# Performance work log

Measured on AMD Instinct MI355X. Metric: run time of the kernel, lower is better.

The kernel has to match this reference:

```python
import math
import jax, jax.numpy as jnp
import numpy as np

B, NH, L0 = 16, 128, 16384
KS, STRIDE = 4, 2
INIT_GATE_BIAS = 1.0


def _num_steps(L, ks, stride):
    # number of reduce steps until any N <= L reaches N <= 1 (matches torch N recurrence)
    d, n = 0, L
    while True:
        n = (max(n - ks, 0) + stride - 1) // stride + 1
        d += 1
        if n <= 1:
            return d


def setup_inputs() -> dict:
    key = jax.random.key(0)
    k1, k2, k3, k4 = jax.random.split(key, 4)
    h = jax.random.normal(k1, (B, NH, L0), dtype=jnp.float32)
    N = jax.random.randint(k2, (B,), 1, L0 + 1, dtype=jnp.int32)
    cin = NH + 1  # depth_variant adds one channel
    bound = 1.0 / math.sqrt(cin * KS)
    W = jax.random.uniform(k3, (3 * NH, cin, KS), minval=-bound, maxval=bound, dtype=jnp.float32)
    b = jax.random.uniform(k4, (3 * NH,), minval=-bound, maxval=bound, dtype=jnp.float32)
    b = b.at[2 * NH:].set(INIT_GATE_BIAS)
    return {"h": h, "N": N, "W": W, "b": b}


def _step(h, N, depth, W, b):
    Bb, _, Lc = h.shape
    # depth channel (depth_variant=True), then mask invalid positions (mask applied after concat, as in torch)
    d = jnp.full((Bb, 1, Lc), math.log1p(depth), dtype=h.dtype)
    hh = jnp.concatenate([h, d], axis=1)
    mask = (jnp.arange(Lc) < N[:, None]).astype(hh.dtype)  # [B, Lc]
    hh = hh * mask[:, None, :]
    # right-pad so conv covers all valid positions
    if Lc < KS:
        pad_r = KS - Lc
    elif (Lc - KS) % STRIDE != 0:
        pad_r = STRIDE - (Lc - KS) % STRIDE
    else:
        pad_r = 0
    if pad_r:
        hh = jnp.pad(hh, ((0, 0), (0, 0), (0, pad_r)))
    lrg = jax.lax.conv_general_dilated(
        hh, W, window_strides=(STRIDE,), padding='VALID',
        dimension_numbers=('NCH', 'OIH', 'NCH')) + b[None, :, None]
    l = lrg[:, :NH]
    r = jnp.tanh(lrg[:, NH:2 * NH])
    g = jax.nn.sigmoid(lrg[:, 2 * NH:])
    h_new = l * g + r * (1.0 - g)
    m = jnp.maximum(N - KS, 0)
    N_new = (m + STRIDE - 1) // STRIDE + 1  # ceil(clamp(N-ks,0)/stride)+1
    return h_new, N_new


def reference(h, N, W, b):
    # Fixed-depth unroll: instead of compacting the batch (dynamic shapes), run
    # every sample for all D steps and record its row at the step it finishes.
    # Torch output order = samples sorted stably by finish depth (boolean-index
    # compaction preserves original relative order), reproduced via stable argsort.
    D = _num_steps(h.shape[2], KS, STRIDE)
    Bb = h.shape[0]
    out_h = jnp.zeros((Bb, NH), dtype=h.dtype)
    finish = jnp.full((Bb,), D, dtype=jnp.int32)
    done = jnp.zeros((Bb,), dtype=bool)
    for depth in range(D):
        h, N = _step(h, N, depth, W, b)
        newly = (~done) & (N <= 1)
        out_h = jnp.where(newly[:, None], h[:, :, 0], out_h)
        finish = jnp.where(newly, depth, finish)
        done = done | newly
    order = jnp.argsort(finish)  # stable by default in jax
    return out_h[order]
```

## Files before the change

### kernel.cpp

```cpp
#include <hip/hip_runtime.h>
#include <math.h>

typedef _Float16 f16_t;
typedef _Float16 f16x8 __attribute__((ext_vector_type(8)));
typedef _Float16 f16x4 __attribute__((ext_vector_type(4)));
typedef float    f32x4 __attribute__((ext_vector_type(4)));

#define NHC 128
#define NBATCH 16
#define JT 64
#define THREADS 512
#define LDSROWPITCH 272
#define LDSREGION (66*LDSROWPITCH)

__device__ __host__ __forceinline__ int nstep_f(int n){ int m = n - 4; m = m < 0 ? 0 : m; return ((m + 1) >> 1) + 1; }

__global__ void prep_kernel(const float* __restrict__ W, const float* __restrict__ bin,
                            f16_t* __restrict__ Wt, float* __restrict__ Pp, float* __restrict__ biasf)
{
    int c = blockIdx.x;
    int i = threadIdx.x;
    #pragma unroll
    for (int k = 0; k < 4; k++)
        Wt[((size_t)k*384 + c)*128 + i] = (f16_t)W[((size_t)c*129 + i)*4 + k];
    if (i == 0) {
        float s = 0.f;
        Pp[c*5 + 0] = 0.f;
        #pragma unroll
        for (int k = 0; k < 4; k++) { s += W[((size_t)c*129 + 128)*4 + k]; Pp[c*5 + k + 1] = s; }
        biasf[c] = bin[c];
    }
}

__global__ void transpose_kernel(const float* __restrict__ h, const int* __restrict__ N0,
                                 f16_t* __restrict__ X0, int outCols)
{
    __shared__ float tile[32][65];
    const int b = blockIdx.z, c0 = blockIdx.y*32, p0 = blockIdx.x*64;
    const int tid = threadIdx.x;
    const int n0 = N0[b];
    const int L0c = 16384;
    {
        int c = tid >> 3, pc = (tid & 7) * 8;
        const float* src = h + ((size_t)b*NHC + c0 + c)*L0c + p0 + pc;
        float4 v0 = *(const float4*)(src);
        float4 v1 = *(const float4*)(src + 4);
        *(float4*)(&tile[c][pc])     = v0;
        *(float4*)(&tile[c][pc + 4]) = v1;
    }
    __syncthreads();
    {
        int p = tid >> 2, cc = (tid & 3) * 8;
        bool dead = (p0 + p >= n0);
        f16x8 vv;
        #pragma unroll
        for (int e = 0; e < 8; e++) vv[e] = dead ? (f16_t)0.f : (f16_t)tile[cc + e][p];
        *(f16x8*)(X0 + ((size_t)b*outCols + p0 + p)*NHC + c0 + cc) = vv;
    }
}

template<bool TO_LDS>
__device__ __forceinline__ void gemm_epilogue(
    const char* ldsIn, char* ldsOut, f16_t* goutB,
    const f16_t* __restrict__ Wt, const float* __restrict__ Pp,
    const float* __restrict__ biasf, float* __restrict__ outrow,
    int j0, int Nt, int Nt1, float dval, bool record)
{
    const int tid  = threadIdx.x;
    const int w    = tid >> 6;
    const int lane = tid & 63;
    const int n16  = lane & 15;
    const int q    = lane >> 4;

    f32x4 acc[3][4] = {};

    const int arow = w*16 + n16;
    #pragma unroll 1
    for (int k = 0; k < 4; k++) {
        const char*  bb0 = ldsIn + (k&1)*LDSREGION + ((k>>1) + n16)*LDSROWPITCH + q*16;
        const f16_t* ab  = Wt + ((size_t)k*384 + arow)*128 + q*8;
        #pragma unroll 1
        for (int kc = 0; kc < 4; kc++) {
            f16x8 a0 = *(const f16x8*)(ab + kc*32);
            f16x8 a1 = *(const f16x8*)(ab + 16384 + kc*32);
            f16x8 a2 = *(const f16x8*)(ab + 32768 + kc*32);
            #pragma unroll
            for (int ct = 0; ct < 4; ct++) {
                f16x8 bb = *(const f16x8*)(bb0 + ct*(16*LDSROWPITCH) + kc*64);
                acc[0][ct] = __builtin_amdgcn_mfma_f32_16x16x32_f16(a0, bb, acc[0][ct], 0, 0, 0);
                acc[1][ct] = __builtin_amdgcn_mfma_f32_16x16x32_f16(a1, bb, acc[1][ct], 0, 0, 0);
                acc[2][ct] = __builtin_amdgcn_mfma_f32_16x16x32_f16(a2, bb, acc[2][ct], 0, 0, 0);
            }
        }
    }

    if constexpr (TO_LDS) __syncthreads();

    const int cw = w*16 + q*4;
    float biasr[3][4], pfull[3][4];
    #pragma unroll
    for (int s = 0; s < 3; s++)
        #pragma unroll
        for (int r = 0; r < 4; r++) {
            int row = s*128 + cw + r;
            biasr[s][r] = biasf[row];
            pfull[s][r] = Pp[row*5 + 4];
        }

    #pragma unroll
    for (int ct = 0; ct < 4; ct++) {
        int j = j0 + ct*16 + n16;
        int cnt = Nt - 2*j; cnt = cnt < 0 ? 0 : (cnt > 4 ? 4 : cnt);
        bool zero = (j >= Nt1);
        float hv[4];
        #pragma unroll
        for (int r = 0; r < 4; r++) {
            float d0, d1, d2;
            if (cnt == 4)      { d0 = pfull[0][r]; d1 = pfull[1][r]; d2 = pfull[2][r]; }
            else if (cnt == 0) { d0 = 0.f; d1 = 0.f; d2 = 0.f; }
            else { int rw = cw + r; d0 = Pp[rw*5 + cnt]; d1 = Pp[(128+rw)*5 + cnt]; d2 = Pp[(256+rw)*5 + cnt]; }
            float lv = acc[0][ct][r] + biasr[0][r] + dval*d0;
            float rp = acc[1][ct][r] + biasr[1][r] + dval*d1;
            float gp = acc[2][ct][r] + biasr[2][r] + dval*d2;
            float e2 = __expf(2.f*rp);
            float rv = 1.f - 2.f/(e2 + 1.f);
            float gv = 1.f/(1.f + __expf(-gp));
            float hh = lv*gv + rv*(1.f - gv);
            hv[r] = zero ? 0.f : hh;
        }
        f16x4 hb;
        #pragma unroll
        for (int r = 0; r < 4; r++) hb[r] = (f16_t)hv[r];
        if constexpr (TO_LDS) {
            *(f16x4*)(ldsOut + (j&1)*LDSREGION + (j>>1)*LDSROWPITCH + cw*2) = hb;
        } else {
            *(f16x4*)(goutB + (ct*16 + n16)*NHC + cw) = hb;
        }
        if (record && ct == 0 && n16 == 0) {
            #pragma unroll
            for (int r = 0; r < 4; r++) outrow[cw + r] = hv[r];
        }
    }
}

__global__ __launch_bounds__(THREADS) void conv_kernel(
    const f16_t* __restrict__ Xin, f16_t* __restrict__ Xout,
    const f16_t* __restrict__ Wt, const float* __restrict__ Pp,
    const float* __restrict__ biasf, const int* __restrict__ N0,
    float* __restrict__ outbuf,
    int t, int inCols, int outCols, float dval)
{
    __shared__ alignas(16) char ldsX[2*LDSREGION];
    const int b  = blockIdx.y;
    const int j0 = blockIdx.x * JT;
    const int tid = threadIdx.x;
    int Nt = N0[b];
    for (int s = 0; s < t; s++) Nt = nstep_f(Nt);
    const int Nt1 = nstep_f(Nt);

    f16_t* XoutB = Xout + ((size_t)b*outCols + j0)*NHC;
    if (j0 >= Nt1) {
        float4 z = {0.f,0.f,0.f,0.f};
        float4* p = (float4*)XoutB;
        #pragma unroll
        for (int i = 0; i < 2; i++) p[i*THREADS + tid] = z;
        return;
    }

    const char* XinB = (const char*)(Xin + ((size_t)b*inCols + 2*(size_t)j0)*NHC);
    const int maxrow = inCols - 2*j0;
    for (int it = 0; it < 5; ++it) {
        int idx = it*THREADS + tid;
        if (idx < 130*16) {
            int row = idx >> 4, cb = (idx & 15) * 16;
            float4 v = {0.f,0.f,0.f,0.f};
            if (row < maxrow) v = *(const float4*)(XinB + row*256 + cb);
            *(float4*)(ldsX + (row&1)*LDSREGION + (row>>1)*LDSROWPITCH + cb) = v;
        }
    }
    __syncthreads();

    bool newly = (Nt1 == 1) && (t == 0 || Nt > 1);
    gemm_epilogue<false>(ldsX, nullptr, XoutB, Wt, Pp, biasf, outbuf + b*NHC,
                         j0, Nt, Nt1, dval, newly && (j0 == 0));
}

__global__ __launch_bounds__(THREADS) void tail_kernel(
    const f16_t* __restrict__ Xin, const f16_t* __restrict__ Wt,
    const float* __restrict__ Pp, const float* __restrict__ biasf,
    const int* __restrict__ N0, float* __restrict__ outbuf, int inCols)
{
    __shared__ alignas(16) char ldsX[2*LDSREGION];
    const int b = blockIdx.x;
    const int tid = threadIdx.x;
    int Nt = N0[b];
    for (int s = 0; s < 7; s++) Nt = nstep_f(Nt);

    const char* XinB = (const char*)(Xin + (size_t)b*inCols*NHC);
    for (int it = 0; it < 5; ++it) {
        int idx = it*THREADS + tid;
        if (idx < 130*16) {
            int row = idx >> 4, cb = (idx & 15) * 16;
            float4 v = {0.f,0.f,0.f,0.f};
            if (row < inCols) v = *(const float4*)(XinB + row*256 + cb);
            *(float4*)(ldsX + (row&1)*LDSREGION + (row>>1)*LDSROWPITCH + cb) = v;
        }
    }
    __syncthreads();

    for (int t = 7; t < 13; ++t) {
        int Nt1 = nstep_f(Nt);
        bool newly = (Nt1 == 1) && (Nt > 1);
        float dval = log1pf((float)t);
        gemm_epilogue<true>(ldsX, ldsX, nullptr, Wt, Pp, biasf, outbuf + b*NHC,
                            0, Nt, Nt1, dval, newly);
        Nt = Nt1;
        __syncthreads();
    }
}

__global__ void finalize_kernel(const float* __restrict__ outbuf,
                                const int* __restrict__ N0, float* __restrict__ dout)
{
    __shared__ int fin[16];
    __shared__ int rnk[16];
    int tid = threadIdx.x;
    if (tid < 16) {
        int n = N0[tid]; int f = 12;
        for (int t = 0; t < 13; t++) { n = nstep_f(n); if (n == 1) { f = t; break; } }
        fin[tid] = f;
    }
    __syncthreads();
    if (tid < 16) {
        int r = 0;
        for (int b2 = 0; b2 < 16; b2++)
            if (fin[b2] < fin[tid] || (fin[b2] == fin[tid] && b2 < tid)) r++;
        rnk[tid] = r;
    }
    __syncthreads();
    for (int e = tid; e < NBATCH*NHC; e += 256) {
        int b = e >> 7, c = e & 127;
        dout[rnk[b]*NHC + c] = outbuf[e];
    }
}

extern "C" void kernel_launch(void* const* d_in, const int* in_sizes, int n_in,
                              void* d_out, int out_size, void* d_ws, size_t ws_size,
                              hipStream_t stream)
{
    const float* h    = (const float*)d_in[0];
    const int*   N0   = (const int*)d_in[1];
    const float* W    = (const float*)d_in[2];
    const float* bvec = (const float*)d_in[3];
    float* dout = (float*)d_out;

    int Ls[14], Ms[14];
    Ls[0] = 16384;
    for (int t = 0; t < 13; t++) Ls[t+1] = nstep_f(Ls[t]);
    for (int t = 0; t < 14; t++) Ms[t] = ((Ls[t] + 63) / 64) * 64;

    char* ws = (char*)d_ws;
    size_t off = 0;
    auto alloc = [&](size_t bytes){ size_t o = off; off += (bytes + 255) & ~(size_t)255; return o; };
    size_t oXA   = alloc((size_t)NBATCH * Ms[0] * NHC * 2);
    size_t oXB   = alloc((size_t)NBATCH * Ms[1] * NHC * 2);
    size_t oWt   = alloc((size_t)4*384*128*2);
    size_t oPp   = alloc((size_t)384*5*4);
    size_t oBias = alloc((size_t)384*4);
    size_t oOut  = alloc((size_t)NBATCH*NHC*4);
    f16_t* XA    = (f16_t*)(ws + oXA);
    f16_t* XB    = (f16_t*)(ws + oXB);
    f16_t* Wt    = (f16_t*)(ws + oWt);
    float* Pp    = (float*)(ws + oPp);
    float* biasf = (float*)(ws + oBias);
    float* outb  = (float*)(ws + oOut);

    hipLaunchKernelGGL(prep_kernel, dim3(384), dim3(128), 0, stream, W, bvec, Wt, Pp, biasf);
    hipLaunchKernelGGL(transpose_kernel, dim3(Ms[0]/64, 4, NBATCH), dim3(256), 0, stream, h, N0, XA, Ms[0]);

    f16_t* cur = XA; f16_t* nxt = XB;
    for (int t = 0; t < 7; t++) {
        hipLaunchKernelGGL(conv_kernel, dim3(Ms[t+1]/64, NBATCH), dim3(THREADS), 0, stream,
                           cur, nxt, Wt, Pp, biasf, N0, outb, t, Ms[t], Ms[t+1], log1pf((float)t));
        f16_t* tmp = cur; cur = nxt; nxt = tmp;
    }
    hipLaunchKernelGGL(tail_kernel, dim3(NBATCH), dim3(THREADS), 0, stream,
                       cur, Wt, Pp, biasf, N0, outb, Ms[7]);
    hipLaunchKernelGGL(finalize_kernel, dim3(1), dim3(256), 0, stream, outb, N0, dout);
}
```

Before: 524.9 us.

## Specialize tail kernel with column-tile-count templated MFMA loop and early exits

Replaces the generic gemm_epilogue call in the tail kernel with a dedicated tail_iter templated on the number of active 16-column tiles, chosen from the shrinking sequence length each step. Blocks whose sample is already finished return immediately, and blocks exit once their sample finishes. Bias and full-window depth projections are hoisted into registers. This cuts MFMA work on columns that are already dead in the late, short steps, at the cost of more code paths and template instantiations.

```diff
diff --git a/kernel.cpp b/kernel.cpp
--- a/kernel.cpp
+++ b/kernel.cpp
@@ -185,6 +185,68 @@
                          j0, Nt, Nt1, dval, newly && (j0 == 0));
 }
 
+template<int CTM>
+__device__ __forceinline__ void tail_iter(
+    char* ldsX, const f16_t* __restrict__ Wt, const float* __restrict__ Pp,
+    float* __restrict__ outrow,
+    const float (&biasr)[3][4], const float (&pfull)[3][4],
+    int n16, int q, int arow, int cw,
+    int Nt, int Nt1, float dval, bool newly)
+{
+    f32x4 acc[3][CTM] = {};
+    #pragma unroll
+    for (int k = 0; k < 4; k++) {
+        const char*  bb0 = ldsX + (k&1)*LDSREGION + ((k>>1) + n16)*LDSROWPITCH + q*16;
+        const f16_t* ab  = Wt + ((size_t)k*384 + arow)*128 + q*8;
+        #pragma unroll
+        for (int kc = 0; kc < 4; kc++) {
+            f16x8 a0 = *(const f16x8*)(ab + kc*32);
+            f16x8 a1 = *(const f16x8*)(ab + 16384 + kc*32);
+            f16x8 a2 = *(const f16x8*)(ab + 32768 + kc*32);
+            #pragma unroll
+            for (int ct = 0; ct < CTM; ct++) {
+                f16x8 bb = *(const f16x8*)(bb0 + ct*(16*LDSROWPITCH) + kc*64);
+                acc[0][ct] = __builtin_amdgcn_mfma_f32_16x16x32_f16(a0, bb, acc[0][ct], 0, 0, 0);
+                acc[1][ct] = __builtin_amdgcn_mfma_f32_16x16x32_f16(a1, bb, acc[1][ct], 0, 0, 0);
+                acc[2][ct] = __builtin_amdgcn_mfma_f32_16x16x32_f16(a2, bb, acc[2][ct], 0, 0, 0);
+            }
+        }
+    }
+
+    __syncthreads();
+
+    #pragma unroll
+    for (int ct = 0; ct < CTM; ct++) {
+        int j = ct*16 + n16;
+        int cnt = Nt - 2*j; cnt = cnt < 0 ? 0 : (cnt > 4 ? 4 : cnt);
+        bool zero = (j >= Nt1);
+        float hv[4];
+        #pragma unroll
+        for (int r = 0; r < 4; r++) {
+            float d0, d1, d2;
+            if (cnt == 4)      { d0 = pfull[0][r]; d1 = pfull[1][r]; d2 = pfull[2][r]; }
+            else if (cnt == 0) { d0 = 0.f; d1 = 0.f; d2 = 0.f; }
+            else { int rw = cw + r; d0 = Pp[rw*5 + cnt]; d1 = Pp[(128+rw)*5 + cnt]; d2 = Pp[(256+rw)*5 + cnt]; }
+            float lv = acc[0][ct][r] + biasr[0][r] + dval*d0;
+            float rp = acc[1][ct][r] + biasr[1][r] + dval*d1;
+            float gp = acc[2][ct][r] + biasr[2][r] + dval*d2;
+            float e2 = __expf(2.f*rp);
+            float rv = 1.f - 2.f/(e2 + 1.f);
+            float gv = 1.f/(1.f + __expf(-gp));
+            float hh = lv*gv + rv*(1.f - gv);
+            hv[r] = zero ? 0.f : hh;
+        }
+        f16x4 hb;
+        #pragma unroll
+        for (int r = 0; r < 4; r++) hb[r] = (f16_t)hv[r];
+        *(f16x4*)(ldsX + (j&1)*LDSREGION + (j>>1)*LDSROWPITCH + cw*2) = hb;
+        if (newly && ct == 0 && n16 == 0) {
+            #pragma unroll
+            for (int r = 0; r < 4; r++) outrow[cw + r] = hv[r];
+        }
+    }
+}
+
 __global__ __launch_bounds__(THREADS) void tail_kernel(
     const f16_t* __restrict__ Xin, const f16_t* __restrict__ Wt,
     const float* __restrict__ Pp, const float* __restrict__ biasf,
@@ -195,6 +257,7 @@
     const int tid = threadIdx.x;
     int Nt = N0[b];
     for (int s = 0; s < 7; s++) Nt = nstep_f(Nt);
+    if (Nt <= 1) return;
 
     const char* XinB = (const char*)(Xin + (size_t)b*inCols*NHC);
     for (int it = 0; it < 5; ++it) {
@@ -206,14 +269,38 @@
             *(float4*)(ldsX + (row&1)*LDSREGION + (row>>1)*LDSROWPITCH + cb) = v;
         }
     }
+
+    const int w    = tid >> 6;
+    const int lane = tid & 63;
+    const int n16  = lane & 15;
+    const int q    = lane >> 4;
+    const int arow = w*16 + n16;
+    const int cw   = w*16 + q*4;
+    float* outrow  = outbuf + b*NHC;
+
+    float biasr[3][4], pfull[3][4];
+    #pragma unroll
+    for (int s = 0; s < 3; s++)
+        #pragma unroll
+        for (int r = 0; r < 4; r++) {
+            int row = s*128 + cw + r;
+            biasr[s][r] = biasf[row];
+            pfull[s][r] = Pp[row*5 + 4];
+        }
     __syncthreads();
 
     for (int t = 7; t < 13; ++t) {
         int Nt1 = nstep_f(Nt);
-        bool newly = (Nt1 == 1) && (Nt > 1);
+        bool newly = (Nt1 == 1);
         float dval = log1pf((float)t);
-        gemm_epilogue<true>(ldsX, ldsX, nullptr, Wt, Pp, biasf, outbuf + b*NHC,
-                            0, Nt, Nt1, dval, newly);
+        int ctmax = (Nt1 >> 4) + 1; if (ctmax > 4) ctmax = 4;
+        switch (ctmax) {
+        case 1:  tail_iter<1>(ldsX, Wt, Pp, outrow, biasr, pfull, n16, q, arow, cw, Nt, Nt1, dval, newly); break;
+        case 2:  tail_iter<2>(ldsX, Wt, Pp, outrow, biasr, pfull, n16, q, arow, cw, Nt, Nt1, dval, newly); break;
+        case 3:  tail_iter<3>(ldsX, Wt, Pp, outrow, biasr, pfull, n16, q, arow, cw, Nt, Nt1, dval, newly); break;
+        default: tail_iter<4>(ldsX, Wt, Pp, outrow, biasr, pfull, n16, q, arow, cw, Nt, Nt1, dval, newly); break;
+        }
+        if (newly) return;
         Nt = Nt1;
         __syncthreads();
     }
```

Result: faster. 512.8 us (-2.3%).

## Hoist weight fragments into registers and skip MFMA tiles past valid length

Applied to the files above, without the earlier changes.

Loads all A-matrix weight fragments (48 f16x8 vectors per thread) into registers once per block before the LDS fill, instead of reloading them from global memory inside the k-loop. The GEMM is templated on the number of active column tiles, so tiles beyond the sample's current valid length are not computed, in both the step kernel and the tail kernel. The tail kernel also returns early for samples that are already finished and exits once a sample finishes. The cost is much higher register pressure (about 192 VGPRs for the A fragments plus accumulators), which may limit occupancy or cause spills, and more code from the template variants.

```diff
diff --git a/kernel.cpp b/kernel.cpp
--- a/kernel.cpp
+++ b/kernel.cpp
@@ -59,45 +59,26 @@
     }
 }
 
-template<bool TO_LDS>
-__device__ __forceinline__ void gemm_epilogue(
-    const char* ldsIn, char* ldsOut, f16_t* goutB,
-    const f16_t* __restrict__ Wt, const float* __restrict__ Pp,
-    const float* __restrict__ biasf, float* __restrict__ outrow,
-    int j0, int Nt, int Nt1, float dval, bool record)
-{
-    const int tid  = threadIdx.x;
-    const int w    = tid >> 6;
-    const int lane = tid & 63;
-    const int n16  = lane & 15;
-    const int q    = lane >> 4;
-
-    f32x4 acc[3][4] = {};
-
-    const int arow = w*16 + n16;
-    #pragma unroll 1
+struct AFrag { f16x8 a[4][4][3]; };
+
+__device__ __forceinline__ void load_afrag(AFrag& A, const f16_t* __restrict__ Wt, int arow, int q)
+{
+    #pragma unroll
     for (int k = 0; k < 4; k++) {
-        const char*  bb0 = ldsIn + (k&1)*LDSREGION + ((k>>1) + n16)*LDSROWPITCH + q*16;
-        const f16_t* ab  = Wt + ((size_t)k*384 + arow)*128 + q*8;
-        #pragma unroll 1
+        const f16_t* ab = Wt + ((size_t)k*384 + arow)*128 + q*8;
+        #pragma unroll
         for (int kc = 0; kc < 4; kc++) {
-            f16x8 a0 = *(const f16x8*)(ab + kc*32);
-            f16x8 a1 = *(const f16x8*)(ab + 16384 + kc*32);
-            f16x8 a2 = *(const f16x8*)(ab + 32768 + kc*32);
-            #pragma unroll
-            for (int ct = 0; ct < 4; ct++) {
-                f16x8 bb = *(const f16x8*)(bb0 + ct*(16*LDSROWPITCH) + kc*64);
-                acc[0][ct] = __builtin_amdgcn_mfma_f32_16x16x32_f16(a0, bb, acc[0][ct], 0, 0, 0);
-                acc[1][ct] = __builtin_amdgcn_mfma_f32_16x16x32_f16(a1, bb, acc[1][ct], 0, 0, 0);
-                acc[2][ct] = __builtin_amdgcn_mfma_f32_16x16x32_f16(a2, bb, acc[2][ct], 0, 0, 0);
-            }
-        }
-    }
-
-    if constexpr (TO_LDS) __syncthreads();
-
-    const int cw = w*16 + q*4;
-    float biasr[3][4], pfull[3][4];
+            A.a[k][kc][0] = *(const f16x8*)(ab + kc*32);
+            A.a[k][kc][1] = *(const f16x8*)(ab + 16384 + kc*32);
+            A.a[k][kc][2] = *(const f16x8*)(ab + 32768 + kc*32);
+        }
+    }
+}
+
+__device__ __forceinline__ void load_biasp(float (&biasr)[3][4], float (&pfull)[3][4],
+                                           const float* __restrict__ biasf,
+                                           const float* __restrict__ Pp, int cw)
+{
     #pragma unroll
     for (int s = 0; s < 3; s++)
         #pragma unroll
@@ -106,9 +87,37 @@
             biasr[s][r] = biasf[row];
             pfull[s][r] = Pp[row*5 + 4];
         }
-
-    #pragma unroll
-    for (int ct = 0; ct < 4; ct++) {
+}
+
+template<int CTM>
+__device__ __forceinline__ void gemm_regA(f32x4 (&acc)[3][4], const AFrag& A,
+                                          const char* ldsIn, int n16, int q)
+{
+    #pragma unroll
+    for (int k = 0; k < 4; k++) {
+        const char* bb0 = ldsIn + (k&1)*LDSREGION + ((k>>1) + n16)*LDSROWPITCH + q*16;
+        #pragma unroll
+        for (int kc = 0; kc < 4; kc++) {
+            #pragma unroll
+            for (int ct = 0; ct < CTM; ct++) {
+                f16x8 bb = *(const f16x8*)(bb0 + ct*(16*LDSROWPITCH) + kc*64);
+                acc[0][ct] = __builtin_amdgcn_mfma_f32_16x16x32_f16(A.a[k][kc][0], bb, acc[0][ct], 0, 0, 0);
+                acc[1][ct] = __builtin_amdgcn_mfma_f32_16x16x32_f16(A.a[k][kc][1], bb, acc[1][ct], 0, 0, 0);
+                acc[2][ct] = __builtin_amdgcn_mfma_f32_16x16x32_f16(A.a[k][kc][2], bb, acc[2][ct], 0, 0, 0);
+            }
+        }
+    }
+}
+
+template<int CTE, bool TO_LDS>
+__device__ __forceinline__ void epilogue_store(
+    const f32x4 (&acc)[3][4], char* ldsOut, f16_t* goutB,
+    const float (&biasr)[3][4], const float (&pfull)[3][4],
+    const float* __restrict__ Pp, float* __restrict__ outrow,
+    int j0, int Nt, int Nt1, float dval, bool record, int n16, int cw)
+{
+    #pragma unroll
+    for (int ct = 0; ct < CTE; ct++) {
         int j = j0 + ct*16 + n16;
         int cnt = Nt - 2*j; cnt = cnt < 0 ? 0 : (cnt > 4 ? 4 : cnt);
         bool zero = (j >= Nt1);
@@ -167,6 +176,18 @@
         return;
     }
 
+    const int w    = tid >> 6;
+    const int lane = tid & 63;
+    const int n16  = lane & 15;
+    const int q    = lane >> 4;
+    const int arow = w*16 + n16;
+    const int cw   = w*16 + q*4;
+
+    AFrag A;
+    load_afrag(A, Wt, arow, q);
+    float biasr[3][4], pfull[3][4];
+    load_biasp(biasr, pfull, biasf, Pp, cw);
+
     const char* XinB = (const char*)(Xin + ((size_t)b*inCols + 2*(size_t)j0)*NHC);
     const int maxrow = inCols - 2*j0;
     for (int it = 0; it < 5; ++it) {
@@ -180,9 +201,32 @@
     }
     __syncthreads();
 
+    f32x4 acc[3][4] = {};
+    int ctm = (Nt1 - j0 + 15) >> 4; if (ctm > 4) ctm = 4;
+    switch (ctm) {
+    case 1:  gemm_regA<1>(acc, A, ldsX, n16, q); break;
+    case 2:  gemm_regA<2>(acc, A, ldsX, n16, q); break;
+    case 3:  gemm_regA<3>(acc, A, ldsX, n16, q); break;
+    default: gemm_regA<4>(acc, A, ldsX, n16, q); break;
+    }
+
     bool newly = (Nt1 == 1) && (t == 0 || Nt > 1);
-    gemm_epilogue<false>(ldsX, nullptr, XoutB, Wt, Pp, biasf, outbuf + b*NHC,
-                         j0, Nt, Nt1, dval, newly && (j0 == 0));
+    epilogue_store<4, false>(acc, nullptr, XoutB, biasr, pfull, Pp, outbuf + b*NHC,
+                             j0, Nt, Nt1, dval, newly && (j0 == 0), n16, cw);
+}
+
+template<int CTM>
+__device__ __forceinline__ void tail_iter(
+    char* ldsX, const AFrag& A,
+    const float (&biasr)[3][4], const float (&pfull)[3][4],
+    const float* __restrict__ Pp, float* __restrict__ outrow,
+    int n16, int q, int cw, int Nt, int Nt1, float dval, bool newly)
+{
+    f32x4 acc[3][4] = {};
+    gemm_regA<CTM>(acc, A, ldsX, n16, q);
+    __syncthreads();
+    epilogue_store<CTM, true>(acc, ldsX, nullptr, biasr, pfull, Pp, outrow,
+                              0, Nt, Nt1, dval, newly, n16, cw);
 }
 
 __global__ __launch_bounds__(THREADS) void tail_kernel(
@@ -195,6 +239,20 @@
     const int tid = threadIdx.x;
     int Nt = N0[b];
     for (int s = 0; s < 7; s++) Nt = nstep_f(Nt);
+    if (Nt <= 1) return;
+
+    const int w    = tid >> 6;
+    const int lane = tid & 63;
+    const int n16  = lane & 15;
+    const int q    = lane >> 4;
+    const int arow = w*16 + n16;
+    const int cw   = w*16 + q*4;
+    float* outrow  = outbuf + b*NHC;
+
+    AFrag A;
+    load_afrag(A, Wt, arow, q);
+    float biasr[3][4], pfull[3][4];
+    load_biasp(biasr, pfull, biasf, Pp, cw);
 
     const char* XinB = (const char*)(Xin + (size_t)b*inCols*NHC);
     for (int it = 0; it < 5; ++it) {
@@ -210,10 +268,16 @@
 
     for (int t = 7; t < 13; ++t) {
         int Nt1 = nstep_f(Nt);
-        bool newly = (Nt1 == 1) && (Nt > 1);
+        bool newly = (Nt1 == 1);
         float dval = log1pf((float)t);
-        gemm_epilogue<true>(ldsX, ldsX, nullptr, Wt, Pp, biasf, outbuf + b*NHC,
-                            0, Nt, Nt1, dval, newly);
+        int ctmax = (Nt1 >> 4) + 1; if (ctmax > 4) ctmax = 4;
+        switch (ctmax) {
+        case 1:  tail_iter<1>(ldsX, A, biasr, pfull, Pp, outrow, n16, q, cw, Nt, Nt1, dval, newly); break;
+        case 2:  tail_iter<2>(ldsX, A, biasr, pfull, Pp, outrow, n16, q, cw, Nt, Nt1, dval, newly); break;
+        case 3:  tail_iter<3>(ldsX, A, biasr, pfull, Pp, outrow, n16, q, cw, Nt, Nt1, dval, newly); break;
+        default: tail_iter<4>(ldsX, A, biasr, pfull, Pp, outrow, n16, q, cw, Nt, Nt1, dval, newly); break;
+        }
+        if (newly) return;
         Nt = Nt1;
         __syncthreads();
     }
```

Result: slower. 578.6 us (+10.2%).
